# Performance work log

Hardware: AMD Instinct MI355X
Metric: run time of the kernel (lower is better)

The kernel has to match this reference:

```python
import jax, jax.numpy as jnp
import numpy as np

N, E, C, H = 50000, 1600000, 128, 8


def setup_inputs() -> dict:
    key = jax.random.key(0)
    k1, k2, k3, k4, k5 = jax.random.split(key, 5)
    x = jax.random.normal(k1, (N, C), jnp.float32)
    row = jax.random.randint(k2, (E,), 0, N, dtype=jnp.int32)
    col = jax.random.randint(k3, (E,), 0, N, dtype=jnp.int32)
    # ensure no self loops so remove_self_loops is a static no-op
    col = jnp.where(row == col, (col + 1) % N, col)
    edge_index = jnp.stack([row, col])
    edge_attr = jax.random.normal(k4, (E,), jnp.float32)
    # Linear(2*C, H) params
    W = jax.random.normal(k5, (2 * C, H), jnp.float32) / np.sqrt(2.0 * C)
    b = jnp.zeros((H,), jnp.float32)
    return {"x": x, "edge_index": edge_index, "edge_attr": edge_attr, "W": W, "b": b}


def reference(x, edge_index, edge_attr, W, b):
    n, c = x.shape
    # add self loops (inputs contain none); PyG fill_value=1 for edge weight
    loop = jnp.arange(n, dtype=edge_index.dtype)
    row = jnp.concatenate([edge_index[0], loop])  # [E+N]
    col = jnp.concatenate([edge_index[1], loop])
    ea = jnp.concatenate([edge_attr, jnp.ones((n,), edge_attr.dtype)])
    # cat([x[row], x[col]]) @ W == x[row] @ W[:C] + x[col] @ W[C:] (avoids 2C concat buffer)
    alpha = x[row] @ W[:c] + x[col] @ W[c:] + b          # [E+N, H]
    alpha = alpha * jnp.abs(ea)[:, None]
    alpha = jax.nn.leaky_relu(alpha, negative_slope=0.2)
    alpha = alpha * 100.0
    # segment softmax grouped by row (PyG softmax)
    m = jax.ops.segment_max(alpha, row, num_segments=n)   # [N, H]
    m = jnp.where(jnp.isfinite(m), m, 0.0)                # guard empty segments
    e = jnp.exp(alpha - m[row])
    s = jax.ops.segment_sum(e, row, num_segments=n)
    alpha = e / (s[row] + 1e-16)
    return alpha, jnp.stack([row, col])
```

## Files before the change

### kernel.cpp

```cpp
#include <hip/hip_runtime.h>

#define NN 50000
#define EE 1600000
#define CC 128
#define HH 8
#define TOT (EE + NN)
#define RPB 64
#define NB  ((NN + RPB - 1) / RPB)
#define CAP 2560
#define BCH 4096
#define NBB ((EE + BCH - 1) / BCH)
#define NIT 8
#define GRIDF 6144
#define SRT 512
#define PREG 5
#define UF 4

typedef unsigned long long ull;

__device__ inline float act(float z) {
    z = (z >= 0.f) ? z : 0.2f * z;
    return z * 100.f;
}

__global__ __launch_bounds__(256) void k_proj(const float* __restrict__ x,
                                              const float* __restrict__ W,
                                              const float* __restrict__ bias,
                                              float* __restrict__ yk,
                                              float* __restrict__ y2,
                                              int* __restrict__ gcur0) {
    if (blockIdx.x == 0) {
        for (int i = threadIdx.x; i < NB; i += 256) gcur0[i] = 0;
    }
    __shared__ float w[2 * CC * HH];
    int tid = threadIdx.x;
    for (int i = tid; i < 2 * CC * HH; i += 256) w[i] = W[i];
    __syncthreads();
    int node = blockIdx.x * 16 + (tid >> 4);
    int j = tid & 15;
    if (node >= NN) return;
    int wofs = (j < 8) ? j : (CC * HH + j - 8);
    const float4* xv = (const float4*)(x + (size_t)node * CC);
    float acc = 0.f;
#pragma unroll 4
    for (int k4 = 0; k4 < CC / 4; ++k4) {
        float4 xx = xv[k4];
        int base = k4 * 32 + wofs;
        acc += xx.x * w[base];
        acc += xx.y * w[base + 8];
        acc += xx.z * w[base + 16];
        acc += xx.w * w[base + 24];
    }
    if (j < 8) yk[(size_t)node * 16 + 2 * j] = acc + bias[j];
    else       y2[(size_t)node * 8 + (j - 8)] = acc;
}

__global__ __launch_bounds__(1024) void k_bin(const int* __restrict__ rowp,
                                              const int* __restrict__ colp,
                                              const float* __restrict__ ea,
                                              int* __restrict__ gcur0,
                                              uint2* __restrict__ pay,
                                              float* __restrict__ oidx) {
    __shared__ int hist[NB];
    __shared__ int lscan[NB];
    __shared__ int lofs[NB];
    __shared__ int gofs[NB];
    __shared__ int wsum[16];
    __shared__ uint2 stage[BCH];
    int t = threadIdx.x;
    int lane = t & 63, wv = t >> 6;
    int base = blockIdx.x * BCH;
    int n = EE - base; if (n > BCH) n = BCH;
    for (int i = t; i < NB; i += 1024) hist[i] = 0;
    __syncthreads();
    for (int i = t; i < n; i += 1024)
        atomicAdd(&hist[rowp[base + i] >> 6], 1);
    __syncthreads();
    int own = (t < NB) ? hist[t] : 0;
    int s = own;
#pragma unroll
    for (int off = 1; off < 64; off <<= 1) {
        int u = __shfl_up(s, off, 64);
        if (lane >= off) s += u;
    }
    if (lane == 63) wsum[wv] = s;
    __syncthreads();
    if (t < 16) {
        int v = wsum[t];
        int ss = v;
#pragma unroll
        for (int off = 1; off < 16; off <<= 1) {
            int u = __shfl_up(ss, off, 16);
            if (t >= off) ss += u;
        }
        wsum[t] = ss - v;
    }
    __syncthreads();
    int ex = s + wsum[wv] - own;
    if (t < NB) {
        lscan[t] = ex;
        lofs[t] = ex;
        gofs[t] = own ? (t * CAP + atomicAdd(&gcur0[t], own)) : 0;
    }
    __syncthreads();
    for (int i = t; i < n; i += 1024) {
        int e = base + i;
        int r = rowp[e];
        int c = colp[e];
        float w = fabsf(ea[e]);
        int bkt = r >> 6;
        int p = atomicAdd(&lofs[bkt], 1);
        stage[p] = make_uint2((unsigned)(r & 63) | ((unsigned)c << 6) |
                              ((unsigned)bkt << 22),
                              __float_as_uint(w));
        __builtin_nontemporal_store((float)r, &oidx[e]);
        __builtin_nontemporal_store((float)c, &oidx[(size_t)TOT + e]);
    }
    __syncthreads();
    for (int i = t; i < n; i += 1024) {
        uint2 v = stage[i];
        int bkt = v.x >> 22;
        int idx = gofs[bkt] + (i - lscan[bkt]);
        if (idx < (bkt + 1) * CAP)
            pay[idx] = v;
    }
}

__global__ __launch_bounds__(SRT) void k_sortrow(const int* __restrict__ gcur0,
                                                 const uint2* __restrict__ pay,
                                                 float* __restrict__ yk,
                                                 const float* __restrict__ y2,
                                                 float* __restrict__ alpha,
                                                 float* __restrict__ oidx) {
    __shared__ int cnt[RPB];
    __shared__ int rstartL[RPB + 1];
    __shared__ int ofs2[RPB];
    __shared__ uint2 stg[CAP];
    int b = blockIdx.x;
    int t = threadIdx.x;
    int s0 = b * CAP;
    int n = gcur0[b];
    if (n > CAP) n = CAP;
    if (t < RPB) cnt[t] = 0;
    __syncthreads();
    uint2 preg[PREG];
#pragma unroll
    for (int k = 0; k < PREG; ++k) {
        int i = t + k * SRT;
        preg[k] = make_uint2(0u, 0u);
        if (i < n) {
            preg[k] = pay[s0 + i];
            atomicAdd(&cnt[preg[k].x & 63], 1);
        }
    }
    __syncthreads();
    if (t < RPB) {
        int v = cnt[t];
        int s = v;
        for (int off = 1; off < 64; off <<= 1) {
            int u = __shfl_up(s, off, 64);
            if (t >= off) s += u;
        }
        int ex = s - v;
        ofs2[t] = ex;
        rstartL[t] = ex;
        if (t == RPB - 1) rstartL[RPB] = s;
    }
    __syncthreads();
#pragma unroll
    for (int k = 0; k < PREG; ++k) {
        int i = t + k * SRT;
        if (i < n) {
            uint2 p = preg[k];
            int rl = p.x & 63;
            int pos = atomicAdd(&ofs2[rl], 1);
            stg[pos] = make_uint2((p.x >> 6) & 0xFFFF, p.y);
        }
    }
    __syncthreads();
    int wv = t >> 6;
    int lane = t & 63;
    int sub = lane >> 3;
    int h = lane & 7;
    int r0 = b * RPB;
    for (int q = 0; q < 8; ++q) {
        int rr = wv * 8 + q;
        int r = r0 + rr;
        if (r >= NN) break;
        int ls = rstartL[rr];
        int ldeg = rstartL[rr + 1] - ls;
        int tot = ldeg + 1;
        float yh = yk[(size_t)r * 16 + 2 * h];
        float y2s = y2[(size_t)r * 8 + h];
        float cache[NIT];
        float mx = -__builtin_inff();
#pragma unroll
        for (int it = 0; it < NIT; ++it) {
            int i = it * 8 + sub;
            float a = -__builtin_inff();
            if (i < tot) {
                if (i < ldeg) {
                    uint2 p = stg[ls + i];
                    a = act((yh + y2[(size_t)p.x * 8 + h]) * __uint_as_float(p.y));
                } else {
                    a = act(yh + y2s);
                }
            }
            cache[it] = a;
            mx = fmaxf(mx, a);
        }
        for (int i = NIT * 8 + sub; i < tot; i += 8) {
            float a;
            if (i < ldeg) {
                uint2 p = stg[ls + i];
                a = act((yh + y2[(size_t)p.x * 8 + h]) * __uint_as_float(p.y));
            } else {
                a = act(yh + y2s);
            }
            mx = fmaxf(mx, a);
        }
        mx = fmaxf(mx, __shfl_xor(mx, 8, 64));
        mx = fmaxf(mx, __shfl_xor(mx, 16, 64));
        mx = fmaxf(mx, __shfl_xor(mx, 32, 64));
        float sum = 0.f;
#pragma unroll
        for (int it = 0; it < NIT; ++it)
            sum += __expf(cache[it] - mx);
        for (int i = NIT * 8 + sub; i < tot; i += 8) {
            float a;
            if (i < ldeg) {
                uint2 p = stg[ls + i];
                a = act((yh + y2[(size_t)p.x * 8 + h]) * __uint_as_float(p.y));
            } else {
                a = act(yh + y2s);
            }
            sum += __expf(a - mx);
        }
        sum += __shfl_xor(sum, 8, 64);
        sum += __shfl_xor(sum, 16, 64);
        sum += __shfl_xor(sum, 32, 64);
        if (sub == 0) {
            float K = mx + __logf(sum + 1e-16f);
            yk[(size_t)r * 16 + 2 * h + 1] = K;
            float os = __expf(act(yh + y2s) - K);
            __builtin_nontemporal_store(os, &alpha[(size_t)(EE + r) * 8 + h]);
            if (h == 0) __builtin_nontemporal_store((float)r, &oidx[EE + r]);
            if (h == 1)
                __builtin_nontemporal_store((float)r, &oidx[(size_t)TOT + EE + r]);
        }
    }
}

__global__ __launch_bounds__(256) void k_final(const int* __restrict__ rowp,
                                               const int* __restrict__ colp,
                                               const float* __restrict__ ea,
                                               const float* __restrict__ yk,
                                               const float* __restrict__ y2,
                                               float* __restrict__ alpha) {
    int gid = blockIdx.x * 256 + threadIdx.x;
    int h = gid & 7;
    int g0 = gid >> 3;
    const int stride = (GRIDF * 256) >> 3;
    for (int e0 = g0; e0 < EE; e0 += UF * stride) {
        int rr[UF], cc[UF]; float ww[UF]; bool hv[UF];
#pragma unroll
        for (int u = 0; u < UF; ++u) {
            int e = e0 + u * stride;
            hv[u] = e < EE;
            rr[u] = 0; cc[u] = 0; ww[u] = 0.f;
            if (hv[u]) {
                rr[u] = rowp[e];
                cc[u] = colp[e];
                ww[u] = fabsf(ea[e]);
            }
        }
        float yv[UF], Kv[UF], vb[UF];
#pragma unroll
        for (int u = 0; u < UF; ++u) {
            yv[u] = 0.f; Kv[u] = 0.f; vb[u] = 0.f;
            if (hv[u]) {
                float2 ykv = *(const float2*)&yk[(size_t)rr[u] * 16 + 2 * h];
                yv[u] = ykv.x;
                Kv[u] = ykv.y;
                vb[u] = y2[(size_t)cc[u] * 8 + h];
            }
        }
#pragma unroll
        for (int u = 0; u < UF; ++u) {
            if (hv[u]) {
                int e = e0 + u * stride;
                float o = __expf(act((yv[u] + vb[u]) * ww[u]) - Kv[u]);
                __builtin_nontemporal_store(o, &alpha[(size_t)e * 8 + h]);
            }
        }
    }
}

extern "C" void kernel_launch(void* const* d_in, const int* in_sizes, int n_in,
                              void* d_out, int out_size, void* d_ws, size_t ws_size,
                              hipStream_t stream) {
    const float* x    = (const float*)d_in[0];
    const int*   rowp = (const int*)d_in[1];
    const int*   colp = rowp + EE;
    const float* ea   = (const float*)d_in[2];
    const float* W    = (const float*)d_in[3];
    const float* bias = (const float*)d_in[4];

    float* out_alpha = (float*)d_out;
    float* out_idx   = out_alpha + (size_t)TOT * 8;

    float*  yk     = (float*)d_ws;
    float*  y2     = yk + (size_t)NN * 16;
    uint2*  pay    = (uint2*)(y2 + (size_t)NN * 8);
    int*    gcur0  = (int*)(pay + (size_t)NB * CAP);

    k_proj<<<(NN * 16 + 255) / 256, 256, 0, stream>>>(x, W, bias, yk, y2, gcur0);
    k_bin<<<NBB, 1024, 0, stream>>>(rowp, colp, ea, gcur0, pay, out_idx);
    k_sortrow<<<NB, SRT, 0, stream>>>(gcur0, pay, yk, y2, out_alpha, out_idx);
    k_final<<<GRIDF, 256, 0, stream>>>(rowp, colp, ea, yk, y2, out_alpha);
}
```

Baseline: 96.20 us.

## Merge projection and edge binning into one heterogeneous launch

The node projection kernel and the edge-binning kernel are combined into a single launch whose blocks branch by index: the first NBB blocks bin edges and the rest compute projections, with shared memory unioned between the two roles. The bucket-counter zeroing moves from the projection kernel to a hipMemsetAsync so that binning blocks never depend on projection blocks. This removes one kernel launch and the serial gap between two independent stages so they can overlap on the device. In exchange, projection blocks now run at 1024 threads each, and the union sizes shared memory for the binning layout, which may limit occupancy for projection blocks.

Measured after the change: 98.13 us. 2.0% more time.

```diff
diff --git a/kernel.cpp b/kernel.cpp
--- a/kernel.cpp
+++ b/kernel.cpp
@@ -10,6 +10,7 @@
 #define CAP 2560
 #define BCH 4096
 #define NBB ((EE + BCH - 1) / BCH)
+#define NPB ((NN + 63) / 64)
 #define NIT 8
 #define GRIDF 6144
 #define SRT 512
@@ -23,84 +24,85 @@
     return z * 100.f;
 }
 
-__global__ __launch_bounds__(256) void k_proj(const float* __restrict__ x,
-                                              const float* __restrict__ W,
-                                              const float* __restrict__ bias,
-                                              float* __restrict__ yk,
-                                              float* __restrict__ y2,
-                                              int* __restrict__ gcur0) {
-    if (blockIdx.x == 0) {
-        for (int i = threadIdx.x; i < NB; i += 256) gcur0[i] = 0;
-    }
-    __shared__ float w[2 * CC * HH];
-    int tid = threadIdx.x;
-    for (int i = tid; i < 2 * CC * HH; i += 256) w[i] = W[i];
-    __syncthreads();
-    int node = blockIdx.x * 16 + (tid >> 4);
-    int j = tid & 15;
-    if (node >= NN) return;
-    int wofs = (j < 8) ? j : (CC * HH + j - 8);
-    const float4* xv = (const float4*)(x + (size_t)node * CC);
-    float acc = 0.f;
+__global__ __launch_bounds__(1024) void k_projbin(const float* __restrict__ x,
+                                                  const float* __restrict__ W,
+                                                  const float* __restrict__ bias,
+                                                  float* __restrict__ yk,
+                                                  float* __restrict__ y2,
+                                                  const int* __restrict__ rowp,
+                                                  const int* __restrict__ colp,
+                                                  const float* __restrict__ ea,
+                                                  int* __restrict__ gcur0,
+                                                  uint2* __restrict__ pay,
+                                                  float* __restrict__ oidx) {
+    __shared__ union {
+        float w[2 * CC * HH];
+        struct {
+            int hist[NB];
+            int lscan[NB];
+            int lofs[NB];
+            int gofs[NB];
+            int wsum[16];
+            uint2 stage[BCH];
+        } b;
+    } u;
+    int t = threadIdx.x;
+    if (blockIdx.x >= NBB) {
+        int pb = blockIdx.x - NBB;
+        for (int i = t; i < 2 * CC * HH; i += 1024) u.w[i] = W[i];
+        __syncthreads();
+        int node = pb * 64 + (t >> 4);
+        int j = t & 15;
+        if (node >= NN) return;
+        int wofs = (j < 8) ? j : (CC * HH + j - 8);
+        const float4* xv = (const float4*)(x + (size_t)node * CC);
+        float acc = 0.f;
 #pragma unroll 4
-    for (int k4 = 0; k4 < CC / 4; ++k4) {
-        float4 xx = xv[k4];
-        int base = k4 * 32 + wofs;
-        acc += xx.x * w[base];
-        acc += xx.y * w[base + 8];
-        acc += xx.z * w[base + 16];
-        acc += xx.w * w[base + 24];
-    }
-    if (j < 8) yk[(size_t)node * 16 + 2 * j] = acc + bias[j];
-    else       y2[(size_t)node * 8 + (j - 8)] = acc;
-}
-
-__global__ __launch_bounds__(1024) void k_bin(const int* __restrict__ rowp,
-                                              const int* __restrict__ colp,
-                                              const float* __restrict__ ea,
-                                              int* __restrict__ gcur0,
-                                              uint2* __restrict__ pay,
-                                              float* __restrict__ oidx) {
-    __shared__ int hist[NB];
-    __shared__ int lscan[NB];
-    __shared__ int lofs[NB];
-    __shared__ int gofs[NB];
-    __shared__ int wsum[16];
-    __shared__ uint2 stage[BCH];
-    int t = threadIdx.x;
+        for (int k4 = 0; k4 < CC / 4; ++k4) {
+            float4 xx = xv[k4];
+            int base = k4 * 32 + wofs;
+            acc += xx.x * u.w[base];
+            acc += xx.y * u.w[base + 8];
+            acc += xx.z * u.w[base + 16];
+            acc += xx.w * u.w[base + 24];
+        }
+        if (j < 8) yk[(size_t)node * 16 + 2 * j] = acc + bias[j];
+        else       y2[(size_t)node * 8 + (j - 8)] = acc;
+        return;
+    }
     int lane = t & 63, wv = t >> 6;
     int base = blockIdx.x * BCH;
     int n = EE - base; if (n > BCH) n = BCH;
-    for (int i = t; i < NB; i += 1024) hist[i] = 0;
+    for (int i = t; i < NB; i += 1024) u.b.hist[i] = 0;
     __syncthreads();
     for (int i = t; i < n; i += 1024)
-        atomicAdd(&hist[rowp[base + i] >> 6], 1);
-    __syncthreads();
-    int own = (t < NB) ? hist[t] : 0;
+        atomicAdd(&u.b.hist[rowp[base + i] >> 6], 1);
+    __syncthreads();
+    int own = (t < NB) ? u.b.hist[t] : 0;
     int s = own;
 #pragma unroll
     for (int off = 1; off < 64; off <<= 1) {
-        int u = __shfl_up(s, off, 64);
-        if (lane >= off) s += u;
-    }
-    if (lane == 63) wsum[wv] = s;
+        int uu = __shfl_up(s, off, 64);
+        if (lane >= off) s += uu;
+    }
+    if (lane == 63) u.b.wsum[wv] = s;
     __syncthreads();
     if (t < 16) {
-        int v = wsum[t];
+        int v = u.b.wsum[t];
         int ss = v;
 #pragma unroll
         for (int off = 1; off < 16; off <<= 1) {
-            int u = __shfl_up(ss, off, 16);
-            if (t >= off) ss += u;
-        }
-        wsum[t] = ss - v;
-    }
-    __syncthreads();
-    int ex = s + wsum[wv] - own;
+            int uu = __shfl_up(ss, off, 16);
+            if (t >= off) ss += uu;
+        }
+        u.b.wsum[t] = ss - v;
+    }
+    __syncthreads();
+    int ex = s + u.b.wsum[wv] - own;
     if (t < NB) {
-        lscan[t] = ex;
-        lofs[t] = ex;
-        gofs[t] = own ? (t * CAP + atomicAdd(&gcur0[t], own)) : 0;
+        u.b.lscan[t] = ex;
+        u.b.lofs[t] = ex;
+        u.b.gofs[t] = own ? (t * CAP + atomicAdd(&gcur0[t], own)) : 0;
     }
     __syncthreads();
     for (int i = t; i < n; i += 1024) {
@@ -109,18 +111,18 @@
         int c = colp[e];
         float w = fabsf(ea[e]);
         int bkt = r >> 6;
-        int p = atomicAdd(&lofs[bkt], 1);
-        stage[p] = make_uint2((unsigned)(r & 63) | ((unsigned)c << 6) |
-                              ((unsigned)bkt << 22),
-                              __float_as_uint(w));
+        int p = atomicAdd(&u.b.lofs[bkt], 1);
+        u.b.stage[p] = make_uint2((unsigned)(r & 63) | ((unsigned)c << 6) |
+                                  ((unsigned)bkt << 22),
+                                  __float_as_uint(w));
         __builtin_nontemporal_store((float)r, &oidx[e]);
         __builtin_nontemporal_store((float)c, &oidx[(size_t)TOT + e]);
     }
     __syncthreads();
     for (int i = t; i < n; i += 1024) {
-        uint2 v = stage[i];
+        uint2 v = u.b.stage[i];
         int bkt = v.x >> 22;
-        int idx = gofs[bkt] + (i - lscan[bkt]);
+        int idx = u.b.gofs[bkt] + (i - u.b.lscan[bkt]);
         if (idx < (bkt + 1) * CAP)
             pay[idx] = v;
     }
@@ -314,8 +316,9 @@
     uint2*  pay    = (uint2*)(y2 + (size_t)NN * 8);
     int*    gcur0  = (int*)(pay + (size_t)NB * CAP);
 
-    k_proj<<<(NN * 16 + 255) / 256, 256, 0, stream>>>(x, W, bias, yk, y2, gcur0);
-    k_bin<<<NBB, 1024, 0, stream>>>(rowp, colp, ea, gcur0, pay, out_idx);
+    hipMemsetAsync(gcur0, 0, NB * sizeof(int), stream);
+    k_projbin<<<NBB + NPB, 1024, 0, stream>>>(x, W, bias, yk, y2,
+                                              rowp, colp, ea, gcur0, pay, out_idx);
     k_sortrow<<<NB, SRT, 0, stream>>>(gcur0, pay, yk, y2, out_alpha, out_idx);
     k_final<<<GRIDF, 256, 0, stream>>>(rowp, colp, ea, yk, y2, out_alpha);
 }
```
